# Performance work log

Hardware: AMD Instinct MI355X
Metric: run time of the kernel (lower is better)

## Reference

```python
import jax, jax.numpy as jnp
import numpy as np

WS = 8          # window size
NUM_HEADS = 12


def setup_inputs() -> dict:
    key = jax.random.key(0)
    k1, k2, k3 = jax.random.split(key, 3)
    B, N, C = 16, 4096, 384
    x = jax.random.normal(k1, (B, N, C), dtype=jnp.float32)
    # torch Linear weights stored as [in, out] so forward is x @ W
    qkv_w = jax.random.normal(k2, (C, 3 * C), dtype=jnp.float32) * (C ** -0.5)
    proj_w = jax.random.normal(k3, (C, C), dtype=jnp.float32) * (C ** -0.5)
    proj_b = jnp.zeros((C,), dtype=jnp.float32)
    return {"x": x, "qkv_w": qkv_w, "proj_w": proj_w, "proj_b": proj_b}


def reference(x, qkv_w, proj_w, proj_b):
    B, N, C = x.shape
    H = W = int(np.sqrt(N))
    hg, wg = H // WS, W // WS
    G = hg * wg
    nh = NUM_HEADS
    hd = C // nh
    scale = hd ** -0.5

    # window partition: [B, N, C] -> [B, hg, wg, ws, ws, C]
    xw = x.reshape(B, hg, WS, wg, WS, C).transpose(0, 1, 3, 2, 4, 5)
    xw = xw.reshape(B, G, WS * WS, C)

    # qkv projection -> [3, B, G, nh, ws*ws, hd]
    qkv = (xw @ qkv_w).reshape(B, G, WS * WS, 3, nh, hd)
    qkv = qkv.transpose(3, 0, 1, 4, 2, 5)
    q, k, v = qkv[0], qkv[1], qkv[2]

    attn = jnp.einsum('bgnqd,bgnkd->bgnqk', q, k) * scale
    attn = jax.nn.softmax(attn, axis=-1)
    out = jnp.einsum('bgnqk,bgnkd->bgnqd', attn, v)

    # merge heads and reverse window partition
    out = out.transpose(0, 1, 3, 2, 4).reshape(B, hg, wg, WS, WS, C)
    out = out.transpose(0, 1, 3, 2, 4, 5).reshape(B, N, C)

    return out @ proj_w + proj_b
```

## Files before the change

### kernel.cpp

```cpp
#include <hip/hip_runtime.h>
#include <stdint.h>

typedef unsigned short ushort_t;
typedef __bf16 bf16x8 __attribute__((ext_vector_type(8)));
typedef float floatx4 __attribute__((ext_vector_type(4)));
typedef unsigned short ushort8 __attribute__((ext_vector_type(8)));

__device__ __forceinline__ ushort_t f2b(float f) {
  union { float f; unsigned u; } v; v.f = f;
  unsigned r = v.u + 0x7fffu + ((v.u >> 16) & 1u);
  return (ushort_t)(r >> 16);
}
__device__ __forceinline__ ushort_t b2u(float f) {
  union { __bf16 b; ushort_t u; } v; v.b = (__bf16)f; return v.u;
}
__device__ __forceinline__ bf16x8 cvt8(const float* p) {
  floatx4 f0 = *(const floatx4*)p;
  floatx4 f1 = *(const floatx4*)(p + 4);
  union { bf16x8 v; __bf16 e[8]; } u;
#pragma unroll
  for (int j = 0; j < 4; ++j) u.e[j] = (__bf16)f0[j];
#pragma unroll
  for (int j = 0; j < 4; ++j) u.e[4 + j] = (__bf16)f1[j];
  return u.v;
}

__device__ __forceinline__ void async16(const ushort_t* g, ushort_t* l) {
  __builtin_amdgcn_global_load_lds(
      (const __attribute__((address_space(1))) void*)g,
      (__attribute__((address_space(3))) void*)l, 16, 0, 0);
}

__global__ __launch_bounds__(256) void cvt_x(const float* __restrict__ src,
                                             ushort_t* __restrict__ dst, int n8) {
  int i = blockIdx.x * 256 + threadIdx.x;
  if (i < n8) *(bf16x8*)&dst[(size_t)i * 8] = cvt8(src + (size_t)i * 8);
}

__global__ void transpose_k(const float* __restrict__ src,
                            ushort_t* __restrict__ dst, int R, int Cc) {
  int idx = blockIdx.x * 256 + threadIdx.x;
  if (idx < R * Cc) {
    int r = idx / Cc, c = idx % Cc;
    dst[(size_t)c * R + r] = f2b(src[idx]);
  }
}

template <int C_F32>
__global__ __launch_bounds__(256) void gemm_bt(
    const ushort_t* __restrict__ A, int lda,
    const ushort_t* __restrict__ Bt,
    const float* __restrict__ bias, void* __restrict__ C_,
    int M, int N, int K) {
  __shared__ __align__(16) ushort_t As[128 * 32];
  __shared__ __align__(16) ushort_t Bs[128 * 32];
  const int t = threadIdx.x;
  const int n0 = blockIdx.x << 7;
  const int m0 = blockIdx.y << 7;
  const int w = t >> 6, lane = t & 63;
  const int wy = (w >> 1) << 6;
  const int wx = (w & 1) << 6;
  const int l15 = lane & 15;
  const int q8 = (lane >> 4) << 3;
  const int quad4 = (lane >> 4) << 2;

  floatx4 acc[4][4] = {};

  const int srow = t >> 2;
  const int scol = (t & 3) << 3;
  const ushort_t* gA = A + (size_t)(m0 + srow) * lda + scol;
  const ushort_t* gB = Bt + (size_t)(n0 + srow) * K + scol;
  const size_t rstepA = (size_t)64 * lda;
  const size_t rstepB = (size_t)64 * K;

  for (int k0 = 0; k0 < K; k0 += 32) {
    __syncthreads();
    async16(gA + k0, &As[t * 8]);
    async16(gA + rstepA + k0, &As[2048 + t * 8]);
    async16(gB + k0, &Bs[t * 8]);
    async16(gB + rstepB + k0, &Bs[2048 + t * 8]);
    __syncthreads();
    bf16x8 af[4], bfr[4];
#pragma unroll
    for (int i = 0; i < 4; ++i)
      af[i] = *(const bf16x8*)&As[(wy + i * 16 + l15) * 32 + q8];
#pragma unroll
    for (int j = 0; j < 4; ++j)
      bfr[j] = *(const bf16x8*)&Bs[(wx + j * 16 + l15) * 32 + q8];
#pragma unroll
    for (int i = 0; i < 4; ++i)
#pragma unroll
      for (int j = 0; j < 4; ++j)
        acc[i][j] = __builtin_amdgcn_mfma_f32_16x16x32_bf16(
            af[i], bfr[j], acc[i][j], 0, 0, 0);
  }

  float bv[4] = {0.f, 0.f, 0.f, 0.f};
  if (bias != nullptr) {
#pragma unroll
    for (int j = 0; j < 4; ++j) bv[j] = bias[n0 + wx + j * 16 + l15];
  }
#pragma unroll
  for (int i = 0; i < 4; ++i) {
#pragma unroll
    for (int r = 0; r < 4; ++r) {
      size_t row = (size_t)(m0 + wy + i * 16 + quad4 + r);
      if (C_F32) {
        float* cp = (float*)C_ + row * N + (n0 + wx + l15);
#pragma unroll
        for (int j = 0; j < 4; ++j) cp[j * 16] = acc[i][j][r] + bv[j];
      } else {
        ushort_t* cp = (ushort_t*)C_ + row * N + (n0 + wx + l15);
#pragma unroll
        for (int j = 0; j < 4; ++j) cp[j * 16] = f2b(acc[i][j][r] + bv[j]);
      }
    }
  }
}

__global__ __launch_bounds__(256, 2) void win_attn(
    const ushort_t* __restrict__ QKV, ushort_t* __restrict__ O, int ostride) {
  __shared__ __align__(16) ushort_t Plds[4][64 * 40];
  __shared__ __align__(16) ushort_t Vt[4][32 * 72];
  const int blk = blockIdx.x;
  const int b = blk >> 6, g = blk & 63;
  const int gy = g >> 3, gx = g & 7;
  const int t = threadIdx.x, w = t >> 6, lane = t & 63;
  const int l15 = lane & 15, quad = lane >> 4;
  const int q8 = quad << 3, quad4 = quad << 2;
  const size_t bbase = (size_t)b * 4096 + (size_t)(gy * 8) * 64 + gx * 8;
  const float scale = 0.17677669529663687f;

  bf16x8 ones;
  {
    union { bf16x8 v; __bf16 e[8]; } u;
#pragma unroll
    for (int j = 0; j < 8; ++j) u.e[j] = (__bf16)1.0f;
    ones = u.v;
  }

  for (int hi = 0; hi < 3; ++hi) {
    const int h = w * 3 + hi;
    const size_t hq = (size_t)h * 32;

    {
      size_t row = bbase + (size_t)(lane >> 3) * 64 + (lane & 7);
      const ushort_t* vp = QKV + row * 1152 + 768 + hq;
#pragma unroll
      for (int i = 0; i < 4; ++i) {
        ushort8 vv = *(const ushort8*)(vp + i * 8);
#pragma unroll
        for (int j = 0; j < 8; ++j) Vt[w][(i * 8 + j) * 72 + lane] = vv[j];
      }
    }

    bf16x8 qf[4], kf[4];
#pragma unroll
    for (int i = 0; i < 4; ++i) {
      int tok = i * 16 + l15;
      size_t row = bbase + (size_t)(tok >> 3) * 64 + (tok & 7);
      qf[i] = *(const bf16x8*)(QKV + row * 1152 + hq + q8);
      kf[i] = *(const bf16x8*)(QKV + row * 1152 + 384 + hq + q8);
    }

    floatx4 s[4][4] = {};
#pragma unroll
    for (int i = 0; i < 4; ++i)
#pragma unroll
      for (int j = 0; j < 4; ++j)
        s[i][j] = __builtin_amdgcn_mfma_f32_16x16x32_bf16(
            qf[i], kf[j], s[i][j], 0, 0, 0);

    floatx4 o[4][2] = {};
    floatx4 osum[4] = {};
#pragma unroll
    for (int ks = 0; ks < 2; ++ks) {
#pragma unroll
      for (int i = 0; i < 4; ++i) {
#pragma unroll
        for (int r = 0; r < 4; ++r) {
          float p0 = __expf(s[i][2 * ks][r] * scale);
          float p1 = __expf(s[i][2 * ks + 1][r] * scale);
          int pr = (i * 16 + quad4 + r) * 40 + l15;
          Plds[w][pr] = b2u(p0);
          Plds[w][pr + 16] = b2u(p1);
        }
      }
      bf16x8 pf[4], vf[2];
#pragma unroll
      for (int i = 0; i < 4; ++i)
        pf[i] = *(const bf16x8*)&Plds[w][(i * 16 + l15) * 40 + q8];
#pragma unroll
      for (int j = 0; j < 2; ++j)
        vf[j] = *(const bf16x8*)&Vt[w][(j * 16 + l15) * 72 + ks * 32 + q8];
#pragma unroll
      for (int i = 0; i < 4; ++i) {
#pragma unroll
        for (int j = 0; j < 2; ++j)
          o[i][j] = __builtin_amdgcn_mfma_f32_16x16x32_bf16(
              pf[i], vf[j], o[i][j], 0, 0, 0);
        osum[i] = __builtin_amdgcn_mfma_f32_16x16x32_bf16(
            pf[i], ones, osum[i], 0, 0, 0);
      }
    }

#pragma unroll
    for (int i = 0; i < 4; ++i) {
#pragma unroll
      for (int r = 0; r < 4; ++r) {
        int tok = i * 16 + quad4 + r;
        size_t row = bbase + (size_t)(tok >> 3) * 64 + (tok & 7);
        float inv = 1.0f / osum[i][r];
        ushort_t* op = O + row * (size_t)ostride + hq;
#pragma unroll
        for (int j = 0; j < 2; ++j) op[j * 16 + l15] = b2u(o[i][j][r] * inv);
      }
    }
  }
}

extern "C" void kernel_launch(void* const* d_in, const int* in_sizes, int n_in,
                              void* d_out, int out_size, void* d_ws, size_t ws_size,
                              hipStream_t stream) {
  const float* x      = (const float*)d_in[0];
  const float* qkv_w  = (const float*)d_in[1];
  const float* proj_w = (const float*)d_in[2];
  const float* proj_b = (const float*)d_in[3];
  float* out = (float*)d_out;

  const int M = 16 * 4096;
  const size_t need =
      ((size_t)M * 1152 + (size_t)M * 384 + 1152 * 384 + 384 * 384) * 2;
  if (ws_size < need) return;

  ushort_t* qkv    = (ushort_t*)d_ws;
  ushort_t* xb     = qkv + (size_t)M * 1152;
  ushort_t* qkvwT  = xb + (size_t)M * 384;
  ushort_t* projwT = qkvwT + (size_t)1152 * 384;

  cvt_x<<<(M * 384 / 8 + 255) / 256, 256, 0, stream>>>(x, xb, M * 384 / 8);
  transpose_k<<<(384 * 1152 + 255) / 256, 256, 0, stream>>>(qkv_w, qkvwT, 384, 1152);
  transpose_k<<<(384 * 384 + 255) / 256, 256, 0, stream>>>(proj_w, projwT, 384, 384);

  gemm_bt<0><<<dim3(1152 / 128, M / 128), 256, 0, stream>>>(
      xb, 384, qkvwT, nullptr, qkv, M, 1152, 384);

  win_attn<<<16 * 64, 256, 0, stream>>>(qkv, qkv, 1152);

  gemm_bt<1><<<dim3(384 / 128, M / 128), 256, 0, stream>>>(
      qkv, 1152, projwT, proj_b, out, M, 384, 384);
}
```

Before: 370.3 us.

## Deepen GEMM K-tile to 64 with XOR-swizzled LDS and XCD-aware block remap

The GEMM kernel now stages a 64-wide K slice per iteration, which halves the number of barrier pairs. It stores the A and B tiles in LDS with an XOR swizzle of 16-byte chunks so that the MFMA operand reads avoid bank conflicts. The launch grid becomes 1D, and block indices are remapped so that consecutive tiles are spread across the 8 XCDs for better L2 locality. LDS use doubles to 32KB per block, which could reduce occupancy.

```diff
diff --git a/kernel.cpp b/kernel.cpp
--- a/kernel.cpp
+++ b/kernel.cpp
@@ -52,47 +52,59 @@
     const ushort_t* __restrict__ Bt,
     const float* __restrict__ bias, void* __restrict__ C_,
     int M, int N, int K) {
-  __shared__ __align__(16) ushort_t As[128 * 32];
-  __shared__ __align__(16) ushort_t Bs[128 * 32];
+  __shared__ __align__(16) ushort_t As[128 * 64];
+  __shared__ __align__(16) ushort_t Bs[128 * 64];
   const int t = threadIdx.x;
-  const int n0 = blockIdx.x << 7;
-  const int m0 = blockIdx.y << 7;
+
+  const int nwg = gridDim.x;
+  const int per = nwg >> 3;
+  const int swz = (blockIdx.x & 7) * per + (blockIdx.x >> 3);
+  const int ntn = N >> 7;
+  const int m0 = (swz / ntn) << 7;
+  const int n0 = (swz % ntn) << 7;
+
   const int w = t >> 6, lane = t & 63;
   const int wy = (w >> 1) << 6;
   const int wx = (w & 1) << 6;
   const int l15 = lane & 15;
-  const int q8 = (lane >> 4) << 3;
-  const int quad4 = (lane >> 4) << 2;
+  const int quad = lane >> 4;
+  const int quad4 = quad << 2;
 
   floatx4 acc[4][4] = {};
 
-  const int srow = t >> 2;
-  const int scol = (t & 3) << 3;
-  const ushort_t* gA = A + (size_t)(m0 + srow) * lda + scol;
-  const ushort_t* gB = Bt + (size_t)(n0 + srow) * K + scol;
-  const size_t rstepA = (size_t)64 * lda;
-  const size_t rstepB = (size_t)64 * K;
-
-  for (int k0 = 0; k0 < K; k0 += 32) {
+  const int srow = t >> 3;
+  const int sc = (((t & 7) ^ (srow & 7)) << 3);
+  const ushort_t* gA = A + (size_t)(m0 + srow) * lda + sc;
+  const ushort_t* gB = Bt + (size_t)(n0 + srow) * K + sc;
+
+  for (int k0 = 0; k0 < K; k0 += 64) {
     __syncthreads();
-    async16(gA + k0, &As[t * 8]);
-    async16(gA + rstepA + k0, &As[2048 + t * 8]);
-    async16(gB + k0, &Bs[t * 8]);
-    async16(gB + rstepB + k0, &Bs[2048 + t * 8]);
+#pragma unroll
+    for (int r4 = 0; r4 < 4; ++r4) {
+      async16(gA + (size_t)r4 * 32 * lda + k0, &As[r4 * 2048 + t * 8]);
+      async16(gB + (size_t)r4 * 32 * K + k0, &Bs[r4 * 2048 + t * 8]);
+    }
     __syncthreads();
-    bf16x8 af[4], bfr[4];
-#pragma unroll
-    for (int i = 0; i < 4; ++i)
-      af[i] = *(const bf16x8*)&As[(wy + i * 16 + l15) * 32 + q8];
-#pragma unroll
-    for (int j = 0; j < 4; ++j)
-      bfr[j] = *(const bf16x8*)&Bs[(wx + j * 16 + l15) * 32 + q8];
-#pragma unroll
-    for (int i = 0; i < 4; ++i)
-#pragma unroll
-      for (int j = 0; j < 4; ++j)
-        acc[i][j] = __builtin_amdgcn_mfma_f32_16x16x32_bf16(
-            af[i], bfr[j], acc[i][j], 0, 0, 0);
+#pragma unroll
+    for (int kk = 0; kk < 2; ++kk) {
+      bf16x8 af[4], bfr[4];
+#pragma unroll
+      for (int i = 0; i < 4; ++i) {
+        int row = wy + i * 16 + l15;
+        af[i] = *(const bf16x8*)&As[row * 64 + ((((kk << 2) | quad) ^ (row & 7)) << 3)];
+      }
+#pragma unroll
+      for (int j = 0; j < 4; ++j) {
+        int row = wx + j * 16 + l15;
+        bfr[j] = *(const bf16x8*)&Bs[row * 64 + ((((kk << 2) | quad) ^ (row & 7)) << 3)];
+      }
+#pragma unroll
+      for (int i = 0; i < 4; ++i)
+#pragma unroll
+        for (int j = 0; j < 4; ++j)
+          acc[i][j] = __builtin_amdgcn_mfma_f32_16x16x32_bf16(
+              af[i], bfr[j], acc[i][j], 0, 0, 0);
+    }
   }
 
   float bv[4] = {0.f, 0.f, 0.f, 0.f};
@@ -242,11 +254,11 @@
   transpose_k<<<(384 * 1152 + 255) / 256, 256, 0, stream>>>(qkv_w, qkvwT, 384, 1152);
   transpose_k<<<(384 * 384 + 255) / 256, 256, 0, stream>>>(proj_w, projwT, 384, 384);
 
-  gemm_bt<0><<<dim3(1152 / 128, M / 128), 256, 0, stream>>>(
+  gemm_bt<0><<<(M / 128) * (1152 / 128), 256, 0, stream>>>(
       xb, 384, qkvwT, nullptr, qkv, M, 1152, 384);
 
   win_attn<<<16 * 64, 256, 0, stream>>>(qkv, qkv, 1152);
 
-  gemm_bt<1><<<dim3(384 / 128, M / 128), 256, 0, stream>>>(
+  gemm_bt<1><<<(M / 128) * (384 / 128), 256, 0, stream>>>(
       qkv, 1152, projwT, proj_b, out, M, 384, 384);
 }
```

After: 337.3 us. 1.1x faster.
